# Kernel tuning notes

Measured on AMD Instinct MI355X. Metric: run time of the kernel, lower is better.

## Reference

```python
import jax, jax.numpy as jnp
import numpy as np

N_NODES = 50000
N_EDGES = 640000
DIMS = [128, 256, 128]


def setup_inputs() -> dict:
    key = jax.random.key(0)
    ks = jax.random.split(key, 8)
    x = jax.random.normal(ks[0], (N_NODES, DIMS[0]), dtype=jnp.float32)
    src = jax.random.randint(ks[1], (N_EDGES,), 0, N_NODES)
    dst = jax.random.randint(ks[2], (N_EDGES,), 0, N_NODES)
    # ensure no pre-existing self loops so add_remaining_self_loops == append all loops
    dst = jnp.where(dst == src, (dst + 1) % N_NODES, dst)
    edge_index = jnp.stack([src, dst]).astype(jnp.int64)
    # SAGEConv lin_l weights (root_weight=False -> only neighbor linear), Kaiming-ish init
    def lin(k, fan_in, fan_out):
        s = 1.0 / np.sqrt(fan_in)
        kw, kb = jax.random.split(k)
        W = jax.random.uniform(kw, (fan_out, fan_in), minval=-s, maxval=s, dtype=jnp.float32)
        b = jax.random.uniform(kb, (fan_out,), minval=-s, maxval=s, dtype=jnp.float32)
        return W, b
    W1, b1 = lin(ks[3], DIMS[0], DIMS[1])
    W2, b2 = lin(ks[4], DIMS[1], DIMS[2])
    logit_scale = jnp.asarray(np.log(1.0 / 0.07), dtype=jnp.float32)
    return {"x": x, "edge_index": edge_index, "W1": W1, "b1": b1,
            "W2": W2, "b2": b2, "logit_scale": logit_scale}


def reference(x, edge_index, W1, b1, W2, b2, logit_scale):
    N = x.shape[0]
    loops = jnp.arange(N, dtype=edge_index.dtype)
    src = jnp.concatenate([edge_index[0], loops])  # add_remaining_self_loops
    dst = jnp.concatenate([edge_index[1], loops])
    deg = jax.ops.segment_sum(jnp.ones_like(dst, dtype=x.dtype), dst, num_segments=N)
    inv_deg = 1.0 / deg  # deg >= 1 thanks to self loops

    def sage_conv(y, W, b):
        # mean aggregation of source features at destination, then linear
        agg = jax.ops.segment_sum(y[src], dst, num_segments=N) * inv_deg[:, None]
        return agg @ W.T + b

    y = jax.nn.relu(sage_conv(x, W1, b1))
    y = sage_conv(y, W2, b2)
    # F.normalize(p=2, dim=-1, eps=1e-12)
    nrm = jnp.maximum(jnp.linalg.norm(y, axis=-1, keepdims=True), 1e-12)
    y = y / nrm
    return y * jnp.exp(logit_scale)
```

## Files before the change

kernel.cpp:

```cpp
#include <hip/hip_runtime.h>
#include <hip/hip_bf16.h>

#define N_NODES 50000
#define NPAD 50048
#define ZROW N_NODES
#define D0 128
#define D1 256
#define D2 128
#define N4 1600000
#define NB4 1601536
#define CAP 128

typedef __attribute__((ext_vector_type(8))) short short8;
typedef __attribute__((ext_vector_type(8))) unsigned short ushort8;
typedef __attribute__((ext_vector_type(4))) float f32x4;

static __device__ __forceinline__ unsigned short f2bf(float f) {
    __hip_bfloat16 h = __float2bfloat16(f);
    return *(unsigned short*)&h;
}
static __device__ __forceinline__ float bf2f(unsigned short u) {
    return __uint_as_float(((unsigned int)u) << 16);
}

__global__ __launch_bounds__(256) void k_prep(const float* __restrict__ x,
                                              unsigned short* __restrict__ x_bf,
                                              int* __restrict__ cursor,
                                              const float* __restrict__ W1,
                                              const float* __restrict__ W2,
                                              unsigned short* __restrict__ W1p,
                                              unsigned short* __restrict__ W2p,
                                              const int* __restrict__ ei32,
                                              int* __restrict__ flag) {
    int idx = blockIdx.x * 256 + threadIdx.x;
    if (idx < N4) {
        float4 v = ((const float4*)x)[idx];
        ushort4 u;
        u.x = f2bf(v.x); u.y = f2bf(v.y); u.z = f2bf(v.z); u.w = f2bf(v.w);
        ((ushort4*)x_bf)[idx] = u;
    } else if (idx < NB4) {
        ushort4 z = {0, 0, 0, 0};
        ((ushort4*)x_bf)[idx] = z;
    }
    if (idx < N_NODES) cursor[idx] = 0;
    if (idx < 2 * D0 * D1) {
        if (idx < D0 * D1) {
            int j = idx & 7, lane = (idx >> 3) & 63, tile = idx >> 9;
            int ct = tile & 15, kt = tile >> 4;
            int k = kt * 32 + (lane >> 4) * 8 + j;
            int n = ct * 16 + (lane & 15);
            W1p[idx] = f2bf(W1[n * D0 + k]);
        } else {
            int i2 = idx - D0 * D1;
            int j = i2 & 7, lane = (i2 >> 3) & 63, tile = i2 >> 9;
            int ct = tile & 7, kt = tile >> 3;
            int k = kt * 32 + (lane >> 4) * 8 + j;
            int n = ct * 16 + (lane & 15);
            W2p[i2] = f2bf(W2[n * D1 + k]);
        }
    }
    if (blockIdx.x == gridDim.x - 1 && threadIdx.x < 64) {
        int lane = threadIdx.x;
        int nz = 0;
#pragma unroll
        for (int k = 0; k < 16; k++) nz += (ei32[2 * (lane * 16 + k) + 1] != 0);
#pragma unroll
        for (int off = 32; off > 0; off >>= 1) nz += __shfl_down(nz, off, 64);
        if (lane == 0) *flag = (nz == 0) ? 1 : 0;
    }
}

__global__ __launch_bounds__(256) void k_bucket(const int* __restrict__ ei,
                                                int* __restrict__ cursor,
                                                int* __restrict__ csr, int E,
                                                const int* __restrict__ flag) {
    int i = blockIdx.x * 256 + threadIdx.x;
    if (2 * i >= E) return;
    int is64 = *flag;
    int s0, d0, s1, d1;
    if (is64) {
        int4 sp = ((const int4*)ei)[i];
        int4 dp = ((const int4*)(ei + 2 * (size_t)E))[i];
        s0 = sp.x; s1 = sp.z; d0 = dp.x; d1 = dp.z;
    } else {
        int2 sp = ((const int2*)ei)[i];
        int2 dp = ((const int2*)(ei + (size_t)E))[i];
        s0 = sp.x; s1 = sp.y; d0 = dp.x; d1 = dp.y;
    }
    int p0 = atomicAdd(&cursor[d0], 1);
    if (p0 < CAP) csr[(size_t)d0 * CAP + p0] = s0;
    if (2 * i + 1 < E) {
        int p1 = atomicAdd(&cursor[d1], 1);
        if (p1 < CAP) csr[(size_t)d1 * CAP + p1] = s1;
    }
}

#define H_LD 260
__global__ __launch_bounds__(256, 4) void k_gmlp(const unsigned short* __restrict__ x_bf,
                                                 const int* __restrict__ csr,
                                                 const int* __restrict__ cursor,
                                                 const unsigned short* __restrict__ W1p,
                                                 const float* __restrict__ b1,
                                                 const unsigned short* __restrict__ W2p,
                                                 unsigned short* __restrict__ t_bf) {
    __shared__ unsigned short sbuf[4][16 * H_LD];
    int tid = threadIdx.x;
    int n0 = blockIdx.x * 64;
    int w = tid >> 6, lane = tid & 63;
    int m = lane & 15, q = lane >> 4;
    unsigned short* wbuf = sbuf[w];

    {
        int h = lane & 15;
        int sub = lane >> 4;
#pragma unroll
        for (int r = 0; r < 4; r++) {
            int lrow = r * 4 + sub;
            int node = n0 + w * 16 + lrow;
            unsigned short* lp = wbuf + lrow * H_LD + h * 8;
            if (node < N_NODES) {
                float a0[8], a1[8];
                ushort8 u = *(const ushort8*)(x_bf + (size_t)node * 128 + h * 8);
#pragma unroll
                for (int t = 0; t < 8; t++) { a0[t] = bf2f(u[t]); a1[t] = 0.f; }
                int dg = cursor[node]; if (dg > CAP) dg = CAP;
                const int* cp = csr + (size_t)node * CAP;
                int jn = (dg + 7) & ~7;
                for (int j = 0; j < jn; j += 8) {
                    int idx[8];
#pragma unroll
                    for (int u8 = 0; u8 < 8; u8++) {
                        int jj = j + u8;
                        idx[u8] = (jj < dg) ? cp[jj] : ZROW;
                    }
                    ushort8 rr[8];
#pragma unroll
                    for (int u8 = 0; u8 < 8; u8++)
                        rr[u8] = *(const ushort8*)(x_bf + (size_t)idx[u8] * 128 + h * 8);
#pragma unroll
                    for (int t = 0; t < 8; t++) {
                        a0[t] += bf2f(rr[0][t]) + bf2f(rr[2][t]) + bf2f(rr[4][t]) + bf2f(rr[6][t]);
                        a1[t] += bf2f(rr[1][t]) + bf2f(rr[3][t]) + bf2f(rr[5][t]) + bf2f(rr[7][t]);
                    }
                }
                float invd = 1.0f / (float)(dg + 1);
                ushort8 o;
#pragma unroll
                for (int t = 0; t < 8; t++) o[t] = f2bf((a0[t] + a1[t]) * invd);
                *(ushort8*)lp = o;
            } else {
                ushort8 z = {0, 0, 0, 0, 0, 0, 0, 0};
                *(ushort8*)lp = z;
            }
        }
    }

    {
        short8 af[4];
        const unsigned short* arow = wbuf + m * H_LD + q * 8;
#pragma unroll
        for (int kt = 0; kt < 4; kt++) af[kt] = *(const short8*)(arow + kt * 32);
#pragma unroll
        for (int ct = 0; ct < 16; ct++) {
            f32x4 acc = {0.f, 0.f, 0.f, 0.f};
#pragma unroll
            for (int kt = 0; kt < 4; kt++) {
                short8 bf = *(const short8*)(W1p + (((kt * 16 + ct) * 64 + lane) << 3));
                acc = __builtin_amdgcn_mfma_f32_16x16x32_bf16(af[kt], bf, acc, 0, 0, 0);
            }
            int c = ct * 16 + m;
            float bias = b1[c];
#pragma unroll
            for (int r = 0; r < 4; r++) {
                float v = fmaxf(acc[r] + bias, 0.0f);
                wbuf[(q * 4 + r) * H_LD + c] = f2bf(v);
            }
        }
    }

    {
        short8 hf[8];
        const unsigned short* hrow = wbuf + m * H_LD + q * 8;
#pragma unroll
        for (int kt = 0; kt < 8; kt++) hf[kt] = *(const short8*)(hrow + kt * 32);
#pragma unroll
        for (int ct = 0; ct < 8; ct++) {
            f32x4 acc = {0.f, 0.f, 0.f, 0.f};
#pragma unroll
            for (int kt = 0; kt < 8; kt++) {
                short8 bf = *(const short8*)(W2p + (((kt * 8 + ct) * 64 + lane) << 3));
                acc = __builtin_amdgcn_mfma_f32_16x16x32_bf16(hf[kt], bf, acc, 0, 0, 0);
            }
            int c = ct * 16 + m;
#pragma unroll
            for (int r = 0; r < 4; r++) {
                int node = n0 + w * 16 + q * 4 + r;
                t_bf[(size_t)node * 128 + c] = (node < N_NODES) ? f2bf(acc[r]) : (unsigned short)0;
            }
        }
    }
}

__global__ __launch_bounds__(256) void k_gather_final(const unsigned short* __restrict__ t,
                                                      const int* __restrict__ csr,
                                                      const int* __restrict__ cursor,
                                                      const float* __restrict__ b2,
                                                      const float* __restrict__ ls,
                                                      float* __restrict__ out) {
    int tid = threadIdx.x;
    int h = tid & 15;
    int node = blockIdx.x * 16 + (tid >> 4);

    float a0[8], a1[8];
    ushort8 u = *(const ushort8*)(t + (size_t)node * 128 + h * 8);
#pragma unroll
    for (int k = 0; k < 8; k++) { a0[k] = bf2f(u[k]); a1[k] = 0.f; }
    int dg = cursor[node]; if (dg > CAP) dg = CAP;
    const int* cp = csr + (size_t)node * CAP;
    int jn = (dg + 7) & ~7;
    for (int j = 0; j < jn; j += 8) {
        int idx[8];
#pragma unroll
        for (int u8 = 0; u8 < 8; u8++) {
            int jj = j + u8;
            idx[u8] = (jj < dg) ? cp[jj] : ZROW;
        }
        ushort8 rr[8];
#pragma unroll
        for (int u8 = 0; u8 < 8; u8++)
            rr[u8] = *(const ushort8*)(t + (size_t)idx[u8] * 128 + h * 8);
#pragma unroll
        for (int k = 0; k < 8; k++) {
            a0[k] += bf2f(rr[0][k]) + bf2f(rr[2][k]) + bf2f(rr[4][k]) + bf2f(rr[6][k]);
            a1[k] += bf2f(rr[1][k]) + bf2f(rr[3][k]) + bf2f(rr[5][k]) + bf2f(rr[7][k]);
        }
    }
    float invd = 1.0f / (float)(dg + 1);
    float4 bb0 = ((const float4*)b2)[h * 2];
    float4 bb1 = ((const float4*)b2)[h * 2 + 1];
    float v[8];
    v[0] = (a0[0] + a1[0]) * invd + bb0.x;
    v[1] = (a0[1] + a1[1]) * invd + bb0.y;
    v[2] = (a0[2] + a1[2]) * invd + bb0.z;
    v[3] = (a0[3] + a1[3]) * invd + bb0.w;
    v[4] = (a0[4] + a1[4]) * invd + bb1.x;
    v[5] = (a0[5] + a1[5]) * invd + bb1.y;
    v[6] = (a0[6] + a1[6]) * invd + bb1.z;
    v[7] = (a0[7] + a1[7]) * invd + bb1.w;

    float s = 0.f;
#pragma unroll
    for (int k = 0; k < 8; k++) s += v[k] * v[k];
#pragma unroll
    for (int msk = 8; msk > 0; msk >>= 1) s += __shfl_xor(s, msk, 64);
    float nrm = fmaxf(sqrtf(s), 1e-12f);
    float scale = expf(ls[0]) / nrm;
    float4 o0, o1;
    o0.x = v[0] * scale; o0.y = v[1] * scale; o0.z = v[2] * scale; o0.w = v[3] * scale;
    o1.x = v[4] * scale; o1.y = v[5] * scale; o1.z = v[6] * scale; o1.w = v[7] * scale;
    float* op = out + (size_t)node * 128 + h * 8;
    *(float4*)(op + 0) = o0;
    *(float4*)(op + 4) = o1;
}

extern "C" void kernel_launch(void* const* d_in, const int* in_sizes, int n_in,
                              void* d_out, int out_size, void* d_ws, size_t ws_size,
                              hipStream_t stream) {
    const float* x  = (const float*)d_in[0];
    const int*   ei = (const int*)d_in[1];
    const float* W1 = (const float*)d_in[2];
    const float* b1 = (const float*)d_in[3];
    const float* W2 = (const float*)d_in[4];
    const float* b2 = (const float*)d_in[5];
    const float* ls = (const float*)d_in[6];
    float* out = (float*)d_out;

    const int E = in_sizes[1] / 2;

    char* ws = (char*)d_ws;
    size_t off = 0;
    auto alloc = [&](size_t bytes) {
        size_t o = off;
        off = (off + bytes + 255) & ~(size_t)255;
        return o;
    };
    int*            flag   = (int*)(ws + alloc(256));
    int*            cursor = (int*)(ws + alloc((size_t)N_NODES * 4));
    int*            csr    = (int*)(ws + alloc((size_t)N_NODES * CAP * 4));
    unsigned short* W1p    = (unsigned short*)(ws + alloc((size_t)D0 * D1 * 2));
    unsigned short* W2p    = (unsigned short*)(ws + alloc((size_t)D1 * D2 * 2));
    unsigned short* x_bf   = (unsigned short*)(ws + alloc((size_t)NPAD * D0 * 2));
    unsigned short* t_bf   = (unsigned short*)(ws + alloc((size_t)NPAD * D2 * 2));

    k_prep<<<(NB4 + 255) / 256, 256, 0, stream>>>(x, x_bf, cursor, W1, W2, W1p, W2p, ei, flag);
    k_bucket<<<(E / 2 + 255) / 256, 256, 0, stream>>>(ei, cursor, csr, E, flag);
    k_gmlp<<<NPAD / 64, 256, 0, stream>>>(x_bf, csr, cursor, W1p, b1, W2p, t_bf);
    k_gather_final<<<N_NODES / 16, 256, 0, stream>>>(t_bf, csr, cursor, b2, ls, out);
}
```

Before: 210.4 us.

## Split fused gather+MLP kernel into separate gather and MLP kernels

Un-fuses the first layer's neighbor mean-aggregation from the MLP kernel. Aggregated features now go to a new bf16 buffer through a standalone gather kernel, and the MLP kernel loads them with plain vector copies. The aim is to free the latency-bound gather from the MLP kernel's launch bounds, LDS footprint and limited block count, so more waves can hide memory latency. The cost is an extra kernel launch plus a global write and read of a 50k×128 bf16 intermediate.

Measured after the change: 219.4 us. 4.3% more time.

```diff
diff --git a/kernel.cpp b/kernel.cpp
--- a/kernel.cpp
+++ b/kernel.cpp
@@ -95,14 +95,56 @@
     }
 }
 
+__global__ __launch_bounds__(256) void k_gather(const unsigned short* __restrict__ x_bf,
+                                                const int* __restrict__ csr,
+                                                const int* __restrict__ cursor,
+                                                unsigned short* __restrict__ a_bf) {
+    int tid = threadIdx.x;
+    int h = tid & 15;
+    int node = blockIdx.x * 16 + (tid >> 4);
+    unsigned short* dstp = a_bf + (size_t)node * 128 + h * 8;
+    if (node >= N_NODES) {
+        ushort8 z = {0, 0, 0, 0, 0, 0, 0, 0};
+        *(ushort8*)dstp = z;
+        return;
+    }
+    float a0[8], a1[8];
+    ushort8 u = *(const ushort8*)(x_bf + (size_t)node * 128 + h * 8);
+#pragma unroll
+    for (int t = 0; t < 8; t++) { a0[t] = bf2f(u[t]); a1[t] = 0.f; }
+    int dg = cursor[node]; if (dg > CAP) dg = CAP;
+    const int* cp = csr + (size_t)node * CAP;
+    int jn = (dg + 7) & ~7;
+    for (int j = 0; j < jn; j += 8) {
+        int idx[8];
+#pragma unroll
+        for (int u8 = 0; u8 < 8; u8++) {
+            int jj = j + u8;
+            idx[u8] = (jj < dg) ? cp[jj] : ZROW;
+        }
+        ushort8 rr[8];
+#pragma unroll
+        for (int u8 = 0; u8 < 8; u8++)
+            rr[u8] = *(const ushort8*)(x_bf + (size_t)idx[u8] * 128 + h * 8);
+#pragma unroll
+        for (int t = 0; t < 8; t++) {
+            a0[t] += bf2f(rr[0][t]) + bf2f(rr[2][t]) + bf2f(rr[4][t]) + bf2f(rr[6][t]);
+            a1[t] += bf2f(rr[1][t]) + bf2f(rr[3][t]) + bf2f(rr[5][t]) + bf2f(rr[7][t]);
+        }
+    }
+    float invd = 1.0f / (float)(dg + 1);
+    ushort8 o;
+#pragma unroll
+    for (int t = 0; t < 8; t++) o[t] = f2bf((a0[t] + a1[t]) * invd);
+    *(ushort8*)dstp = o;
+}
+
 #define H_LD 260
-__global__ __launch_bounds__(256, 4) void k_gmlp(const unsigned short* __restrict__ x_bf,
-                                                 const int* __restrict__ csr,
-                                                 const int* __restrict__ cursor,
-                                                 const unsigned short* __restrict__ W1p,
-                                                 const float* __restrict__ b1,
-                                                 const unsigned short* __restrict__ W2p,
-                                                 unsigned short* __restrict__ t_bf) {
+__global__ __launch_bounds__(256, 4) void k_mlp(const unsigned short* __restrict__ a_bf,
+                                                const unsigned short* __restrict__ W1p,
+                                                const float* __restrict__ b1,
+                                                const unsigned short* __restrict__ W2p,
+                                                unsigned short* __restrict__ t_bf) {
     __shared__ unsigned short sbuf[4][16 * H_LD];
     int tid = threadIdx.x;
     int n0 = blockIdx.x * 64;
@@ -111,48 +153,14 @@
     unsigned short* wbuf = sbuf[w];
 
     {
-        int h = lane & 15;
-        int sub = lane >> 4;
-#pragma unroll
-        for (int r = 0; r < 4; r++) {
-            int lrow = r * 4 + sub;
-            int node = n0 + w * 16 + lrow;
-            unsigned short* lp = wbuf + lrow * H_LD + h * 8;
-            if (node < N_NODES) {
-                float a0[8], a1[8];
-                ushort8 u = *(const ushort8*)(x_bf + (size_t)node * 128 + h * 8);
-#pragma unroll
-                for (int t = 0; t < 8; t++) { a0[t] = bf2f(u[t]); a1[t] = 0.f; }
-                int dg = cursor[node]; if (dg > CAP) dg = CAP;
-                const int* cp = csr + (size_t)node * CAP;
-                int jn = (dg + 7) & ~7;
-                for (int j = 0; j < jn; j += 8) {
-                    int idx[8];
-#pragma unroll
-                    for (int u8 = 0; u8 < 8; u8++) {
-                        int jj = j + u8;
-                        idx[u8] = (jj < dg) ? cp[jj] : ZROW;
-                    }
-                    ushort8 rr[8];
-#pragma unroll
-                    for (int u8 = 0; u8 < 8; u8++)
-                        rr[u8] = *(const ushort8*)(x_bf + (size_t)idx[u8] * 128 + h * 8);
-#pragma unroll
-                    for (int t = 0; t < 8; t++) {
-                        a0[t] += bf2f(rr[0][t]) + bf2f(rr[2][t]) + bf2f(rr[4][t]) + bf2f(rr[6][t]);
-                        a1[t] += bf2f(rr[1][t]) + bf2f(rr[3][t]) + bf2f(rr[5][t]) + bf2f(rr[7][t]);
-                    }
-                }
-                float invd = 1.0f / (float)(dg + 1);
-                ushort8 o;
-#pragma unroll
-                for (int t = 0; t < 8; t++) o[t] = f2bf((a0[t] + a1[t]) * invd);
-                *(ushort8*)lp = o;
-            } else {
-                ushort8 z = {0, 0, 0, 0, 0, 0, 0, 0};
-                *(ushort8*)lp = z;
-            }
-        }
+        int lrow = lane >> 2;
+        int quarter = lane & 3;
+        const unsigned short* g = a_bf + (size_t)(n0 + w * 16 + lrow) * 128 + quarter * 32;
+        unsigned short* l = wbuf + lrow * H_LD + quarter * 32;
+        *(short8*)(l + 0)  = *(const short8*)(g + 0);
+        *(short8*)(l + 8)  = *(const short8*)(g + 8);
+        *(short8*)(l + 16) = *(const short8*)(g + 16);
+        *(short8*)(l + 24) = *(const short8*)(g + 24);
     }
 
     {
@@ -290,10 +298,12 @@
     unsigned short* W1p    = (unsigned short*)(ws + alloc((size_t)D0 * D1 * 2));
     unsigned short* W2p    = (unsigned short*)(ws + alloc((size_t)D1 * D2 * 2));
     unsigned short* x_bf   = (unsigned short*)(ws + alloc((size_t)NPAD * D0 * 2));
+    unsigned short* a_bf   = (unsigned short*)(ws + alloc((size_t)NPAD * D0 * 2));
     unsigned short* t_bf   = (unsigned short*)(ws + alloc((size_t)NPAD * D2 * 2));
 
     k_prep<<<(NB4 + 255) / 256, 256, 0, stream>>>(x, x_bf, cursor, W1, W2, W1p, W2p, ei, flag);
     k_bucket<<<(E / 2 + 255) / 256, 256, 0, stream>>>(ei, cursor, csr, E, flag);
-    k_gmlp<<<NPAD / 64, 256, 0, stream>>>(x_bf, csr, cursor, W1p, b1, W2p, t_bf);
+    k_gather<<<NPAD / 16, 256, 0, stream>>>(x_bf, csr, cursor, a_bf);
+    k_mlp<<<NPAD / 64, 256, 0, stream>>>(a_bf, W1p, b1, W2p, t_bf);
     k_gather_final<<<N_NODES / 16, 256, 0, stream>>>(t_bf, csr, cursor, b2, ls, out);
 }
```
